# Kernel optimization log

Hardware: AMD Instinct MI355X
Metric: run time of the kernel (lower is better)

The kernel has to match this reference:

```python
import jax, jax.numpy as jnp
import numpy as np

B, T, U, D, V = 8, 128, 64, 512, 1024

def setup_inputs() -> dict:
    key = jax.random.key(0)
    k1, k2, k3, k4, k5, k6 = jax.random.split(key, 6)
    source_encodings = jax.random.normal(k1, (B, T, D), dtype=jnp.float32)
    target_encodings = jax.random.normal(k2, (B, U, D), dtype=jnp.float32)
    source_lengths = jax.random.randint(k3, (B,), 1, T + 1, dtype=jnp.int32)
    target_lengths = jax.random.randint(k4, (B,), 1, U + 1, dtype=jnp.int32)
    # Linear(D, V): weight (V, D), bias (V), init like torch default (uniform)
    bound = 1.0 / np.sqrt(D)
    W = jax.random.uniform(k5, (V, D), minval=-bound, maxval=bound, dtype=jnp.float32)
    b = jax.random.uniform(k6, (V,), minval=-bound, maxval=bound, dtype=jnp.float32)
    return {"source_encodings": source_encodings, "source_lengths": source_lengths,
            "target_encodings": target_encodings, "target_lengths": target_lengths,
            "W": W, "b": b}

def reference(source_encodings, source_lengths, target_encodings, target_lengths, W, b):
    # broadcast add: (B,T,1,D) + (B,1,U,D) -> (B,T,U,D)
    joint = source_encodings[:, :, None, :] + target_encodings[:, None, :, :]
    relu_out = jax.nn.relu(joint)
    # linear projection: (B,T,U,D) x (D,V) + b -> (B,T,U,V)
    output = jnp.einsum('btud,vd->btuv', relu_out, W) + b
    return (output, source_lengths, target_lengths)
```

## Files before the change

### kernel.cpp

```cpp
#include <hip/hip_runtime.h>

typedef unsigned short u16;
typedef float  f32x4  __attribute__((ext_vector_type(4)));
typedef int    i32x4  __attribute__((ext_vector_type(4)));
typedef __bf16 bf16x8 __attribute__((ext_vector_type(8)));

#define AS1 __attribute__((address_space(1)))
#define AS3 __attribute__((address_space(3)))

__device__ __forceinline__ void gload_lds16(const void* g, void* l) {
  __builtin_amdgcn_global_load_lds((AS1 void*)g, (AS3 void*)l, 16, 0, 0);
}

constexpr int B_ = 8, T_ = 128, U_ = 64, D_ = 512, V_ = 1024;
constexpr int M_ = B_ * T_ * U_;

__global__ void prep_all(const float* __restrict__ W,
                         const float* __restrict__ src,
                         const float* __restrict__ tgt,
                         const int* __restrict__ sl, const int* __restrict__ tl,
                         u16* __restrict__ Wb, u16* __restrict__ Aw,
                         float* __restrict__ tail) {
  if (blockIdx.x == 0 && threadIdx.x < 16) {
    const int t = threadIdx.x;
    tail[t] = (t < 8) ? (float)sl[t] : (float)tl[t - 8];
  }
  if (blockIdx.x < 256) {
    const int tid = blockIdx.x * 256 + threadIdx.x;
    const int v  = tid >> 6;
    const int cs = tid & 63;
    const float* sp = W + (size_t)v * D_ + cs * 8;
    float4 w0 = *(const float4*)sp;
    float4 w1 = *(const float4*)(sp + 4);
    union { __bf16 h[8]; i32x4 x; } pk;
    pk.h[0] = (__bf16)w0.x; pk.h[1] = (__bf16)w0.y;
    pk.h[2] = (__bf16)w0.z; pk.h[3] = (__bf16)w0.w;
    pk.h[4] = (__bf16)w1.x; pk.h[5] = (__bf16)w1.y;
    pk.h[6] = (__bf16)w1.z; pk.h[7] = (__bf16)w1.w;
    const int dc = (cs >> 3) * 8 + ((cs & 7) ^ (v & 7));
    *(i32x4*)(Wb + (size_t)v * D_ + dc * 8) = pk.x;
  } else {
    const int tid = (blockIdx.x - 256) * 256 + threadIdx.x;
    const int m  = tid >> 6;
    const int cs = tid & 63;
    const int bt = m >> 6;
    const int u  = m & 63;
    const int b  = m >> 13;
    const float* sp = src + (size_t)bt * D_ + cs * 8;
    const float* tp = tgt + ((size_t)b * U_ + u) * D_ + cs * 8;
    float4 s0 = *(const float4*)sp;
    float4 s1 = *(const float4*)(sp + 4);
    float4 t0 = *(const float4*)tp;
    float4 t1 = *(const float4*)(tp + 4);
    union { __bf16 h[8]; i32x4 x; } pk;
    pk.h[0] = (__bf16)fmaxf(s0.x + t0.x, 0.f);
    pk.h[1] = (__bf16)fmaxf(s0.y + t0.y, 0.f);
    pk.h[2] = (__bf16)fmaxf(s0.z + t0.z, 0.f);
    pk.h[3] = (__bf16)fmaxf(s0.w + t0.w, 0.f);
    pk.h[4] = (__bf16)fmaxf(s1.x + t1.x, 0.f);
    pk.h[5] = (__bf16)fmaxf(s1.y + t1.y, 0.f);
    pk.h[6] = (__bf16)fmaxf(s1.z + t1.z, 0.f);
    pk.h[7] = (__bf16)fmaxf(s1.w + t1.w, 0.f);
    const int dc = (cs >> 3) * 8 + ((cs & 7) ^ (m & 7));
    *(i32x4*)(Aw + (size_t)m * D_ + dc * 8) = pk.x;
  }
}

__global__ void tail_k(const int* __restrict__ sl, const int* __restrict__ tl,
                       float* __restrict__ tail) {
  const int t = threadIdx.x;
  if (t < 8)       tail[t] = (float)sl[t];
  else if (t < 16) tail[t] = (float)tl[t - 8];
}

__global__ __launch_bounds__(256, 2) void joiner_gemm_ws(
    const u16* __restrict__ Aw, const u16* __restrict__ Wb,
    const float* __restrict__ bias, float* __restrict__ out)
{
  __shared__ __align__(16) char As[2][16384];
  __shared__ __align__(16) char Bs[2][16384];

  const int tid  = threadIdx.x;
  const int lane = tid & 63;
  const int wid  = tid >> 6;
  const int wgid = blockIdx.x;
  const int xcd  = wgid & 7;
  const int j    = wgid >> 3;
  const int bm   = xcd * 64 + (j >> 3);
  const int bn   = j & 7;
  const int wm   = (wid >> 1) * 64;
  const int wn   = (wid & 1) * 64;

  f32x4 acc[4][4] = {};

  float bv[4];
  #pragma unroll
  for (int ni = 0; ni < 4; ++ni)
    bv[ni] = bias[bn * 128 + wn + ni * 16 + (lane & 15)];

  auto issueA = [&](int kt, int nb) {
    #pragma unroll
    for (int q = 0; q < 4; ++q) {
      const int i   = wid * 4 + q;
      const int row = i * 8 + (lane >> 3);
      const u16* g = Aw + (size_t)(bm * 128 + row) * D_ + kt * 64 + (lane & 7) * 8;
      gload_lds16(g, As[nb] + i * 1024);
    }
  };
  auto issueB = [&](int kt, int nb) {
    #pragma unroll
    for (int q = 0; q < 4; ++q) {
      const int i   = wid * 4 + q;
      const int row = i * 8 + (lane >> 3);
      const u16* g = Wb + (size_t)(bn * 128 + row) * D_ + kt * 64 + (lane & 7) * 8;
      gload_lds16(g, Bs[nb] + i * 1024);
    }
  };

  auto compute = [&](int cb) {
    #pragma unroll
    for (int s = 0; s < 2; ++s) {
      const int kc = s * 4 + (lane >> 4);
      bf16x8 af[4], bg[4];
      #pragma unroll
      for (int mi = 0; mi < 4; ++mi) {
        const int r = wm + mi * 16 + (lane & 15);
        af[mi] = *(const bf16x8*)(As[cb] + r * 128 + ((kc ^ (r & 7)) << 4));
      }
      #pragma unroll
      for (int ni = 0; ni < 4; ++ni) {
        const int n = wn + ni * 16 + (lane & 15);
        bg[ni] = *(const bf16x8*)(Bs[cb] + n * 128 + ((kc ^ (n & 7)) << 4));
      }
      __builtin_amdgcn_s_setprio(1);
      #pragma unroll
      for (int mi = 0; mi < 4; ++mi)
        #pragma unroll
        for (int ni = 0; ni < 4; ++ni)
          acc[mi][ni] = __builtin_amdgcn_mfma_f32_16x16x32_bf16(
              af[mi], bg[ni], acc[mi][ni], 0, 0, 0);
      __builtin_amdgcn_s_setprio(0);
    }
  };

  issueA(0, 0); issueB(0, 0);

  for (int kt = 0; kt < 8; ++kt) {
    const int cur = kt & 1;
    __syncthreads();
    if (kt < 7) { issueA(kt + 1, cur ^ 1); issueB(kt + 1, cur ^ 1); }
    compute(cur);
  }

  const int col = lane & 15;
  const int r4  = (lane >> 4) * 4;
  #pragma unroll
  for (int mi = 0; mi < 4; ++mi) {
    const size_t mrow = (size_t)bm * 128 + wm + mi * 16 + r4;
    float* op0 = out + mrow * V_ + bn * 128 + wn + col;
    #pragma unroll
    for (int ni = 0; ni < 4; ++ni) {
      float* op = op0 + ni * 16;
      const f32x4 v = acc[mi][ni];
      op[0 * V_] = v[0] + bv[ni];
      op[1 * V_] = v[1] + bv[ni];
      op[2 * V_] = v[2] + bv[ni];
      op[3 * V_] = v[3] + bv[ni];
    }
  }
}

__global__ __launch_bounds__(256, 2) void joiner_gemm_f32(
    const float* __restrict__ src, const float* __restrict__ tgt,
    const float* __restrict__ Wf, const float* __restrict__ bias,
    float* __restrict__ out)
{
  __shared__ char As[128 * 128];
  __shared__ char Bs[128 * 128];

  const int tid  = threadIdx.x;
  const int lane = tid & 63;
  const int wid  = tid >> 6;
  const int bn   = blockIdx.x & 7;
  const int bm   = blockIdx.x >> 3;
  const int bt0  = bm * 2;
  const int bb   = bt0 >> 7;
  const int sr0  = tid >> 3;
  const int sc8  = tid & 7;
  const int wm   = (wid >> 1) * 64;
  const int wn   = (wid & 1) * 64;

  f32x4 acc[4][4] = {};

  const float* srcp0 = src + (size_t)bt0 * D_ + sc8 * 8;
  const float* srcp1 = srcp0 + D_;
  const float* tgtp0 = tgt + ((size_t)bb * U_ + sr0) * D_ + sc8 * 8;
  const float* tgtp1 = tgtp0 + (size_t)32 * D_;

  for (int kt = 0; kt < 8; ++kt) {
    const int k0 = kt * 64;
    #pragma unroll
    for (int jj = 0; jj < 4; ++jj) {
      const int vr = sr0 + 32 * jj;
      const float* wp = Wf + (size_t)(bn * 128 + vr) * D_ + k0 + sc8 * 8;
      float4 w0 = *(const float4*)wp;
      float4 w1 = *(const float4*)(wp + 4);
      union { __bf16 h[8]; i32x4 x; } pk;
      pk.h[0] = (__bf16)w0.x; pk.h[1] = (__bf16)w0.y;
      pk.h[2] = (__bf16)w0.z; pk.h[3] = (__bf16)w0.w;
      pk.h[4] = (__bf16)w1.x; pk.h[5] = (__bf16)w1.y;
      pk.h[6] = (__bf16)w1.z; pk.h[7] = (__bf16)w1.w;
      *(i32x4*)(Bs + vr * 128 + ((sc8 ^ (vr & 7)) << 4)) = pk.x;
    }
    float4 s0a = *(const float4*)(srcp0 + k0), s0b = *(const float4*)(srcp0 + k0 + 4);
    float4 s1a = *(const float4*)(srcp1 + k0), s1b = *(const float4*)(srcp1 + k0 + 4);
    float4 t0a = *(const float4*)(tgtp0 + k0), t0b = *(const float4*)(tgtp0 + k0 + 4);
    float4 t1a = *(const float4*)(tgtp1 + k0), t1b = *(const float4*)(tgtp1 + k0 + 4);
    #pragma unroll
    for (int i = 0; i < 2; ++i) {
      const float4 sa = i ? s1a : s0a;
      const float4 sb = i ? s1b : s0b;
      #pragma unroll
      for (int jj = 0; jj < 2; ++jj) {
        const float4 ta = jj ? t1a : t0a;
        const float4 tb = jj ? t1b : t0b;
        const int r = i * 64 + jj * 32 + sr0;
        union { __bf16 h[8]; i32x4 x; } pk;
        pk.h[0] = (__bf16)fmaxf(sa.x + ta.x, 0.f);
        pk.h[1] = (__bf16)fmaxf(sa.y + ta.y, 0.f);
        pk.h[2] = (__bf16)fmaxf(sa.z + ta.z, 0.f);
        pk.h[3] = (__bf16)fmaxf(sa.w + ta.w, 0.f);
        pk.h[4] = (__bf16)fmaxf(sb.x + tb.x, 0.f);
        pk.h[5] = (__bf16)fmaxf(sb.y + tb.y, 0.f);
        pk.h[6] = (__bf16)fmaxf(sb.z + tb.z, 0.f);
        pk.h[7] = (__bf16)fmaxf(sb.w + tb.w, 0.f);
        *(i32x4*)(As + r * 128 + ((sc8 ^ (r & 7)) << 4)) = pk.x;
      }
    }
    __syncthreads();
    #pragma unroll
    for (int s = 0; s < 2; ++s) {
      const int kc = s * 4 + (lane >> 4);
      bf16x8 af[4], bg[4];
      #pragma unroll
      for (int mi = 0; mi < 4; ++mi) {
        const int r = wm + mi * 16 + (lane & 15);
        af[mi] = *(const bf16x8*)(As + r * 128 + ((kc ^ (r & 7)) << 4));
      }
      #pragma unroll
      for (int ni = 0; ni < 4; ++ni) {
        const int n = wn + ni * 16 + (lane & 15);
        bg[ni] = *(const bf16x8*)(Bs + n * 128 + ((kc ^ (n & 7)) << 4));
      }
      #pragma unroll
      for (int mi = 0; mi < 4; ++mi)
        #pragma unroll
        for (int ni = 0; ni < 4; ++ni)
          acc[mi][ni] = __builtin_amdgcn_mfma_f32_16x16x32_bf16(
              af[mi], bg[ni], acc[mi][ni], 0, 0, 0);
    }
    __syncthreads();
  }

  const int col = lane & 15;
  const int r4  = (lane >> 4) * 4;
  float bv[4];
  #pragma unroll
  for (int ni = 0; ni < 4; ++ni) bv[ni] = bias[bn * 128 + wn + ni * 16 + col];
  #pragma unroll
  for (int mi = 0; mi < 4; ++mi) {
    const size_t mrow = (size_t)bm * 128 + wm + mi * 16 + r4;
    float* op0 = out + mrow * V_ + bn * 128 + wn + col;
    #pragma unroll
    for (int ni = 0; ni < 4; ++ni) {
      float* op = op0 + ni * 16;
      const f32x4 v = acc[mi][ni];
      op[0 * V_] = v[0] + bv[ni];
      op[1 * V_] = v[1] + bv[ni];
      op[2 * V_] = v[2] + bv[ni];
      op[3 * V_] = v[3] + bv[ni];
    }
  }
}

extern "C" void kernel_launch(void* const* d_in, const int* in_sizes, int n_in,
                              void* d_out, int out_size, void* d_ws, size_t ws_size,
                              hipStream_t stream) {
  const float* src  = (const float*)d_in[0];
  const int*   sl   = (const int*)d_in[1];
  const float* tgt  = (const float*)d_in[2];
  const int*   tl   = (const int*)d_in[3];
  const float* W    = (const float*)d_in[4];
  const float* bias = (const float*)d_in[5];
  float* out  = (float*)d_out;
  float* tail = out + (size_t)M_ * V_;

  const size_t needW = (size_t)V_ * D_ * sizeof(u16);
  const size_t needA = (size_t)M_ * D_ * sizeof(u16);

  if (ws_size >= needW + needA) {
    u16* Wb = (u16*)d_ws;
    u16* Aw = Wb + (size_t)V_ * D_;
    prep_all<<<256 + M_ * 64 / 256, 256, 0, stream>>>(W, src, tgt, sl, tl, Wb, Aw, tail);
    joiner_gemm_ws<<<(M_ / 128) * (V_ / 128), 256, 0, stream>>>(Aw, Wb, bias, out);
  } else {
    tail_k<<<1, 64, 0, stream>>>(sl, tl, tail);
    joiner_gemm_f32<<<(M_ / 128) * (V_ / 128), 256, 0, stream>>>(src, tgt, W, bias, out);
  }
}
```

Measured before the change: 116.1 us.

## Fuse broadcast-add ReLU into GEMM A-tile load and widen N tile

Removes the materialized bf16 joint activation buffer (M×D) and instead computes relu(src+tgt) on the fly while filling the A tile in LDS. It also widens each block to 512 threads covering 128×256 output tiles, with the bias folded into the accumulator init. The A/B double buffering is dropped in favour of a single buffer with two barriers per k-step. That saves a large write/read round trip through memory, but loses load/compute overlap and re-reads fp32 src/tgt per tile.

```diff
diff --git a/kernel.cpp b/kernel.cpp
--- a/kernel.cpp
+++ b/kernel.cpp
@@ -15,55 +15,26 @@
 constexpr int B_ = 8, T_ = 128, U_ = 64, D_ = 512, V_ = 1024;
 constexpr int M_ = B_ * T_ * U_;
 
-__global__ void prep_all(const float* __restrict__ W,
-                         const float* __restrict__ src,
-                         const float* __restrict__ tgt,
-                         const int* __restrict__ sl, const int* __restrict__ tl,
-                         u16* __restrict__ Wb, u16* __restrict__ Aw,
-                         float* __restrict__ tail) {
+__global__ void prep_w(const float* __restrict__ W,
+                       const int* __restrict__ sl, const int* __restrict__ tl,
+                       u16* __restrict__ Wb, float* __restrict__ tail) {
   if (blockIdx.x == 0 && threadIdx.x < 16) {
     const int t = threadIdx.x;
     tail[t] = (t < 8) ? (float)sl[t] : (float)tl[t - 8];
   }
-  if (blockIdx.x < 256) {
-    const int tid = blockIdx.x * 256 + threadIdx.x;
-    const int v  = tid >> 6;
-    const int cs = tid & 63;
-    const float* sp = W + (size_t)v * D_ + cs * 8;
-    float4 w0 = *(const float4*)sp;
-    float4 w1 = *(const float4*)(sp + 4);
-    union { __bf16 h[8]; i32x4 x; } pk;
-    pk.h[0] = (__bf16)w0.x; pk.h[1] = (__bf16)w0.y;
-    pk.h[2] = (__bf16)w0.z; pk.h[3] = (__bf16)w0.w;
-    pk.h[4] = (__bf16)w1.x; pk.h[5] = (__bf16)w1.y;
-    pk.h[6] = (__bf16)w1.z; pk.h[7] = (__bf16)w1.w;
-    const int dc = (cs >> 3) * 8 + ((cs & 7) ^ (v & 7));
-    *(i32x4*)(Wb + (size_t)v * D_ + dc * 8) = pk.x;
-  } else {
-    const int tid = (blockIdx.x - 256) * 256 + threadIdx.x;
-    const int m  = tid >> 6;
-    const int cs = tid & 63;
-    const int bt = m >> 6;
-    const int u  = m & 63;
-    const int b  = m >> 13;
-    const float* sp = src + (size_t)bt * D_ + cs * 8;
-    const float* tp = tgt + ((size_t)b * U_ + u) * D_ + cs * 8;
-    float4 s0 = *(const float4*)sp;
-    float4 s1 = *(const float4*)(sp + 4);
-    float4 t0 = *(const float4*)tp;
-    float4 t1 = *(const float4*)(tp + 4);
-    union { __bf16 h[8]; i32x4 x; } pk;
-    pk.h[0] = (__bf16)fmaxf(s0.x + t0.x, 0.f);
-    pk.h[1] = (__bf16)fmaxf(s0.y + t0.y, 0.f);
-    pk.h[2] = (__bf16)fmaxf(s0.z + t0.z, 0.f);
-    pk.h[3] = (__bf16)fmaxf(s0.w + t0.w, 0.f);
-    pk.h[4] = (__bf16)fmaxf(s1.x + t1.x, 0.f);
-    pk.h[5] = (__bf16)fmaxf(s1.y + t1.y, 0.f);
-    pk.h[6] = (__bf16)fmaxf(s1.z + t1.z, 0.f);
-    pk.h[7] = (__bf16)fmaxf(s1.w + t1.w, 0.f);
-    const int dc = (cs >> 3) * 8 + ((cs & 7) ^ (m & 7));
-    *(i32x4*)(Aw + (size_t)m * D_ + dc * 8) = pk.x;
-  }
+  const int tid = blockIdx.x * 256 + threadIdx.x;
+  const int v  = tid >> 6;
+  const int cs = tid & 63;
+  const float* sp = W + (size_t)v * D_ + cs * 8;
+  float4 w0 = *(const float4*)sp;
+  float4 w1 = *(const float4*)(sp + 4);
+  union { __bf16 h[8]; i32x4 x; } pk;
+  pk.h[0] = (__bf16)w0.x; pk.h[1] = (__bf16)w0.y;
+  pk.h[2] = (__bf16)w0.z; pk.h[3] = (__bf16)w0.w;
+  pk.h[4] = (__bf16)w1.x; pk.h[5] = (__bf16)w1.y;
+  pk.h[6] = (__bf16)w1.z; pk.h[7] = (__bf16)w1.w;
+  const int dc = (cs >> 3) * 8 + ((cs & 7) ^ (v & 7));
+  *(i32x4*)(Wb + (size_t)v * D_ + dc * 8) = pk.x;
 }
 
 __global__ void tail_k(const int* __restrict__ sl, const int* __restrict__ tl,
@@ -73,51 +44,91 @@
   else if (t < 16) tail[t] = (float)tl[t - 8];
 }
 
-__global__ __launch_bounds__(256, 2) void joiner_gemm_ws(
-    const u16* __restrict__ Aw, const u16* __restrict__ Wb,
-    const float* __restrict__ bias, float* __restrict__ out)
+__global__ __launch_bounds__(512, 4) void joiner_gemm(
+    const float* __restrict__ src, const float* __restrict__ tgt,
+    const u16* __restrict__ Wb, const float* __restrict__ bias,
+    float* __restrict__ out)
 {
-  __shared__ __align__(16) char As[2][16384];
-  __shared__ __align__(16) char Bs[2][16384];
+  __shared__ __align__(16) char As[16384];
+  __shared__ __align__(16) char Bs[32768];
 
   const int tid  = threadIdx.x;
   const int lane = tid & 63;
   const int wid  = tid >> 6;
   const int wgid = blockIdx.x;
   const int xcd  = wgid & 7;
-  const int j    = wgid >> 3;
-  const int bm   = xcd * 64 + (j >> 3);
-  const int bn   = j & 7;
-  const int wm   = (wid >> 1) * 64;
-  const int wn   = (wid & 1) * 64;
-
-  f32x4 acc[4][4] = {};
-
-  float bv[4];
-  #pragma unroll
-  for (int ni = 0; ni < 4; ++ni)
-    bv[ni] = bias[bn * 128 + wn + ni * 16 + (lane & 15)];
-
-  auto issueA = [&](int kt, int nb) {
-    #pragma unroll
-    for (int q = 0; q < 4; ++q) {
-      const int i   = wid * 4 + q;
-      const int row = i * 8 + (lane >> 3);
-      const u16* g = Aw + (size_t)(bm * 128 + row) * D_ + kt * 64 + (lane & 7) * 8;
-      gload_lds16(g, As[nb] + i * 1024);
-    }
-  };
-  auto issueB = [&](int kt, int nb) {
-    #pragma unroll
-    for (int q = 0; q < 4; ++q) {
-      const int i   = wid * 4 + q;
-      const int row = i * 8 + (lane >> 3);
-      const u16* g = Wb + (size_t)(bn * 128 + row) * D_ + kt * 64 + (lane & 7) * 8;
-      gload_lds16(g, Bs[nb] + i * 1024);
-    }
-  };
-
-  auto compute = [&](int cb) {
+  const int idx  = wgid >> 3;
+  const int bn   = xcd >> 1;
+  const int bmi  = idx * 2 + (xcd & 1);
+  const int bt0  = bmi * 2;
+  const int bb   = bmi >> 6;
+  const int wm   = (wid >> 2) * 64;
+  const int wn   = (wid & 3) * 64;
+
+  f32x4 acc[4][4];
+  #pragma unroll
+  for (int ni = 0; ni < 4; ++ni) {
+    const float bv = bias[bn * 256 + wn + ni * 16 + (lane & 15)];
+    #pragma unroll
+    for (int mi = 0; mi < 4; ++mi) acc[mi][ni] = f32x4{bv, bv, bv, bv};
+  }
+
+  const int r0 = tid >> 2;
+  const int c0 = (tid & 3) * 2;
+  const int bt = bt0 + (r0 >> 6);
+  const int u  = r0 & 63;
+  const float* srcp = src + (size_t)bt * D_ + c0 * 8;
+  const float* tgtp = tgt + ((size_t)bb * U_ + u) * D_ + c0 * 8;
+  char* aw0 = As + r0 * 128 + ((c0 ^ (r0 & 7)) << 4);
+  char* aw1 = As + r0 * 128 + (((c0 + 1) ^ (r0 & 7)) << 4);
+
+  const u16* bbase[4];
+  #pragma unroll
+  for (int q = 0; q < 4; ++q) {
+    const int i   = wid * 4 + q;
+    const int row = i * 8 + (lane >> 3);
+    bbase[q] = Wb + (size_t)(bn * 256 + row) * D_ + (lane & 7) * 8;
+  }
+
+  for (int kt = 0; kt < 8; ++kt) {
+    const int k0 = kt * 64;
+    if (kt > 0) __syncthreads();
+
+    #pragma unroll
+    for (int q = 0; q < 4; ++q)
+      gload_lds16(bbase[q] + k0, Bs + (wid * 4 + q) * 1024);
+
+    {
+      float4 s0 = *(const float4*)(srcp + k0);
+      float4 s1 = *(const float4*)(srcp + k0 + 4);
+      float4 s2 = *(const float4*)(srcp + k0 + 8);
+      float4 s3 = *(const float4*)(srcp + k0 + 12);
+      float4 t0 = *(const float4*)(tgtp + k0);
+      float4 t1 = *(const float4*)(tgtp + k0 + 4);
+      float4 t2 = *(const float4*)(tgtp + k0 + 8);
+      float4 t3 = *(const float4*)(tgtp + k0 + 12);
+      union { __bf16 h[8]; i32x4 x; } pk;
+      pk.h[0] = (__bf16)fmaxf(s0.x + t0.x, 0.f);
+      pk.h[1] = (__bf16)fmaxf(s0.y + t0.y, 0.f);
+      pk.h[2] = (__bf16)fmaxf(s0.z + t0.z, 0.f);
+      pk.h[3] = (__bf16)fmaxf(s0.w + t0.w, 0.f);
+      pk.h[4] = (__bf16)fmaxf(s1.x + t1.x, 0.f);
+      pk.h[5] = (__bf16)fmaxf(s1.y + t1.y, 0.f);
+      pk.h[6] = (__bf16)fmaxf(s1.z + t1.z, 0.f);
+      pk.h[7] = (__bf16)fmaxf(s1.w + t1.w, 0.f);
+      *(i32x4*)aw0 = pk.x;
+      pk.h[0] = (__bf16)fmaxf(s2.x + t2.x, 0.f);
+      pk.h[1] = (__bf16)fmaxf(s2.y + t2.y, 0.f);
+      pk.h[2] = (__bf16)fmaxf(s2.z + t2.z, 0.f);
+      pk.h[3] = (__bf16)fmaxf(s2.w + t2.w, 0.f);
+      pk.h[4] = (__bf16)fmaxf(s3.x + t3.x, 0.f);
+      pk.h[5] = (__bf16)fmaxf(s3.y + t3.y, 0.f);
+      pk.h[6] = (__bf16)fmaxf(s3.z + t3.z, 0.f);
+      pk.h[7] = (__bf16)fmaxf(s3.w + t3.w, 0.f);
+      *(i32x4*)aw1 = pk.x;
+    }
+    __syncthreads();
+
     #pragma unroll
     for (int s = 0; s < 2; ++s) {
       const int kc = s * 4 + (lane >> 4);
@@ -125,12 +136,12 @@
       #pragma unroll
       for (int mi = 0; mi < 4; ++mi) {
         const int r = wm + mi * 16 + (lane & 15);
-        af[mi] = *(const bf16x8*)(As[cb] + r * 128 + ((kc ^ (r & 7)) << 4));
+        af[mi] = *(const bf16x8*)(As + r * 128 + ((kc ^ (r & 7)) << 4));
       }
       #pragma unroll
       for (int ni = 0; ni < 4; ++ni) {
         const int n = wn + ni * 16 + (lane & 15);
-        bg[ni] = *(const bf16x8*)(Bs[cb] + n * 128 + ((kc ^ (n & 7)) << 4));
+        bg[ni] = *(const bf16x8*)(Bs + n * 128 + ((kc ^ (n & 7)) << 4));
       }
       __builtin_amdgcn_s_setprio(1);
       #pragma unroll
@@ -141,31 +152,22 @@
               af[mi], bg[ni], acc[mi][ni], 0, 0, 0);
       __builtin_amdgcn_s_setprio(0);
     }
-  };
-
-  issueA(0, 0); issueB(0, 0);
-
-  for (int kt = 0; kt < 8; ++kt) {
-    const int cur = kt & 1;
-    __syncthreads();
-    if (kt < 7) { issueA(kt + 1, cur ^ 1); issueB(kt + 1, cur ^ 1); }
-    compute(cur);
   }
 
   const int col = lane & 15;
   const int r4  = (lane >> 4) * 4;
   #pragma unroll
   for (int mi = 0; mi < 4; ++mi) {
-    const size_t mrow = (size_t)bm * 128 + wm + mi * 16 + r4;
-    float* op0 = out + mrow * V_ + bn * 128 + wn + col;
+    const size_t mrow = (size_t)bmi * 128 + wm + mi * 16 + r4;
+    float* op0 = out + mrow * V_ + bn * 256 + wn + col;
     #pragma unroll
     for (int ni = 0; ni < 4; ++ni) {
       float* op = op0 + ni * 16;
       const f32x4 v = acc[mi][ni];
-      op[0 * V_] = v[0] + bv[ni];
-      op[1 * V_] = v[1] + bv[ni];
-      op[2 * V_] = v[2] + bv[ni];
-      op[3 * V_] = v[3] + bv[ni];
+      op[0 * V_] = v[0];
+      op[1 * V_] = v[1];
+      op[2 * V_] = v[2];
+      op[3 * V_] = v[3];
     }
   }
 }
@@ -295,16 +297,14 @@
   float* out  = (float*)d_out;
   float* tail = out + (size_t)M_ * V_;
 
-  const size_t needW = (size_t)V_ * D_ * sizeof(u16);
-  const size_t needA = (size_t)M_ * D_ * sizeof(u16);
-
-  if (ws_size >= needW + needA) {
+  if (ws_size >= (size_t)V_ * D_ * sizeof(u16)) {
     u16* Wb = (u16*)d_ws;
-    u16* Aw = Wb + (size_t)V_ * D_;
-    prep_all<<<256 + M_ * 64 / 256, 256, 0, stream>>>(W, src, tgt, sl, tl, Wb, Aw, tail);
-    joiner_gemm_ws<<<(M_ / 128) * (V_ / 128), 256, 0, stream>>>(Aw, Wb, bias, out);
+    prep_w<<<256, 256, 0, stream>>>(W, sl, tl, Wb, tail);
+    joiner_gemm<<<(M_ / 128) * (V_ / 256), 512, 0, stream>>>(
+        src, tgt, Wb, bias, out);
   } else {
     tail_k<<<1, 64, 0, stream>>>(sl, tl, tail);
-    joiner_gemm_f32<<<(M_ / 128) * (V_ / 128), 256, 0, stream>>>(src, tgt, W, bias, out);
-  }
-}
+    joiner_gemm_f32<<<(M_ / 128) * (V_ / 128), 256, 0, stream>>>(
+        src, tgt, W, bias, out);
+  }
+}
```

After: 137.4 us. 1.18x slower.

## Fuse broadcast-add ReLU expansion into GEMM A-tile loading instead of materializing

Applied to the files above, without the earlier changes.

Removes the materialized bf16 joint activation buffer (M×D) and instead builds each A tile inside the GEMM from src and tgt rows: registers are prefetched, added, ReLU'd, converted to bf16 and written into a single-buffered swizzled LDS tile. The prep kernel now only converts W. Occupancy is raised to 3 blocks per CU, and block-to-tile mapping drops the XCD-aware swizzle. This avoids writing and rereading a 64 MB intermediate, at the cost of extra barriers, VALU work in the main loop, and a single-buffered A tile that serializes expansion and compute.

```diff
diff --git a/kernel.cpp b/kernel.cpp
--- a/kernel.cpp
+++ b/kernel.cpp
@@ -15,55 +15,26 @@
 constexpr int B_ = 8, T_ = 128, U_ = 64, D_ = 512, V_ = 1024;
 constexpr int M_ = B_ * T_ * U_;
 
-__global__ void prep_all(const float* __restrict__ W,
-                         const float* __restrict__ src,
-                         const float* __restrict__ tgt,
-                         const int* __restrict__ sl, const int* __restrict__ tl,
-                         u16* __restrict__ Wb, u16* __restrict__ Aw,
-                         float* __restrict__ tail) {
+__global__ void prep_w(const float* __restrict__ W,
+                       const int* __restrict__ sl, const int* __restrict__ tl,
+                       u16* __restrict__ Wb, float* __restrict__ tail) {
   if (blockIdx.x == 0 && threadIdx.x < 16) {
     const int t = threadIdx.x;
     tail[t] = (t < 8) ? (float)sl[t] : (float)tl[t - 8];
   }
-  if (blockIdx.x < 256) {
-    const int tid = blockIdx.x * 256 + threadIdx.x;
-    const int v  = tid >> 6;
-    const int cs = tid & 63;
-    const float* sp = W + (size_t)v * D_ + cs * 8;
-    float4 w0 = *(const float4*)sp;
-    float4 w1 = *(const float4*)(sp + 4);
-    union { __bf16 h[8]; i32x4 x; } pk;
-    pk.h[0] = (__bf16)w0.x; pk.h[1] = (__bf16)w0.y;
-    pk.h[2] = (__bf16)w0.z; pk.h[3] = (__bf16)w0.w;
-    pk.h[4] = (__bf16)w1.x; pk.h[5] = (__bf16)w1.y;
-    pk.h[6] = (__bf16)w1.z; pk.h[7] = (__bf16)w1.w;
-    const int dc = (cs >> 3) * 8 + ((cs & 7) ^ (v & 7));
-    *(i32x4*)(Wb + (size_t)v * D_ + dc * 8) = pk.x;
-  } else {
-    const int tid = (blockIdx.x - 256) * 256 + threadIdx.x;
-    const int m  = tid >> 6;
-    const int cs = tid & 63;
-    const int bt = m >> 6;
-    const int u  = m & 63;
-    const int b  = m >> 13;
-    const float* sp = src + (size_t)bt * D_ + cs * 8;
-    const float* tp = tgt + ((size_t)b * U_ + u) * D_ + cs * 8;
-    float4 s0 = *(const float4*)sp;
-    float4 s1 = *(const float4*)(sp + 4);
-    float4 t0 = *(const float4*)tp;
-    float4 t1 = *(const float4*)(tp + 4);
-    union { __bf16 h[8]; i32x4 x; } pk;
-    pk.h[0] = (__bf16)fmaxf(s0.x + t0.x, 0.f);
-    pk.h[1] = (__bf16)fmaxf(s0.y + t0.y, 0.f);
-    pk.h[2] = (__bf16)fmaxf(s0.z + t0.z, 0.f);
-    pk.h[3] = (__bf16)fmaxf(s0.w + t0.w, 0.f);
-    pk.h[4] = (__bf16)fmaxf(s1.x + t1.x, 0.f);
-    pk.h[5] = (__bf16)fmaxf(s1.y + t1.y, 0.f);
-    pk.h[6] = (__bf16)fmaxf(s1.z + t1.z, 0.f);
-    pk.h[7] = (__bf16)fmaxf(s1.w + t1.w, 0.f);
-    const int dc = (cs >> 3) * 8 + ((cs & 7) ^ (m & 7));
-    *(i32x4*)(Aw + (size_t)m * D_ + dc * 8) = pk.x;
-  }
+  const int tid = blockIdx.x * 256 + threadIdx.x;
+  const int v  = tid >> 6;
+  const int cs = tid & 63;
+  const float* sp = W + (size_t)v * D_ + cs * 8;
+  float4 w0 = *(const float4*)sp;
+  float4 w1 = *(const float4*)(sp + 4);
+  union { __bf16 h[8]; i32x4 x; } pk;
+  pk.h[0] = (__bf16)w0.x; pk.h[1] = (__bf16)w0.y;
+  pk.h[2] = (__bf16)w0.z; pk.h[3] = (__bf16)w0.w;
+  pk.h[4] = (__bf16)w1.x; pk.h[5] = (__bf16)w1.y;
+  pk.h[6] = (__bf16)w1.z; pk.h[7] = (__bf16)w1.w;
+  const int dc = (cs >> 3) * 8 + ((cs & 7) ^ (v & 7));
+  *(i32x4*)(Wb + (size_t)v * D_ + dc * 8) = pk.x;
 }
 
 __global__ void tail_k(const int* __restrict__ sl, const int* __restrict__ tl,
@@ -73,47 +44,82 @@
   else if (t < 16) tail[t] = (float)tl[t - 8];
 }
 
-__global__ __launch_bounds__(256, 2) void joiner_gemm_ws(
-    const u16* __restrict__ Aw, const u16* __restrict__ Wb,
-    const float* __restrict__ bias, float* __restrict__ out)
+__global__ __launch_bounds__(256, 3) void joiner_gemm(
+    const float* __restrict__ src, const float* __restrict__ tgt,
+    const u16* __restrict__ Wb, const float* __restrict__ bias,
+    float* __restrict__ out)
 {
-  __shared__ __align__(16) char As[2][16384];
+  __shared__ __align__(16) char As[16384];
   __shared__ __align__(16) char Bs[2][16384];
 
   const int tid  = threadIdx.x;
   const int lane = tid & 63;
   const int wid  = tid >> 6;
-  const int wgid = blockIdx.x;
-  const int xcd  = wgid & 7;
-  const int j    = wgid >> 3;
-  const int bm   = xcd * 64 + (j >> 3);
-  const int bn   = j & 7;
+  const int bn   = blockIdx.x & 7;
+  const int bm   = blockIdx.x >> 3;
+  const int bt0  = bm * 2;
+  const int bb   = bt0 >> 7;
+  const int sr0  = tid >> 3;
+  const int sc8  = tid & 7;
   const int wm   = (wid >> 1) * 64;
   const int wn   = (wid & 1) * 64;
 
   f32x4 acc[4][4] = {};
 
+  const float* srcp0 = src + (size_t)bt0 * D_ + sc8 * 8;
+  const float* srcp1 = srcp0 + D_;
+  const float* tgtp0 = tgt + ((size_t)bb * U_ + sr0) * D_ + sc8 * 8;
+  const float* tgtp1 = tgtp0 + (size_t)32 * D_;
+
   float bv[4];
   #pragma unroll
   for (int ni = 0; ni < 4; ++ni)
     bv[ni] = bias[bn * 128 + wn + ni * 16 + (lane & 15)];
 
-  auto issueA = [&](int kt, int nb) {
-    #pragma unroll
-    for (int q = 0; q < 4; ++q) {
-      const int i   = wid * 4 + q;
-      const int row = i * 8 + (lane >> 3);
-      const u16* g = Aw + (size_t)(bm * 128 + row) * D_ + kt * 64 + (lane & 7) * 8;
-      gload_lds16(g, As[nb] + i * 1024);
-    }
+  const u16* bbase[4];
+  #pragma unroll
+  for (int q = 0; q < 4; ++q) {
+    const int i   = wid * 4 + q;
+    const int row = i * 8 + (lane >> 3);
+    bbase[q] = Wb + (size_t)(bn * 128 + row) * D_ + (lane & 7) * 8;
+  }
+
+  float4 pS0a, pS0b, pS1a, pS1b, pT0a, pT0b, pT1a, pT1b;
+
+  auto loadA = [&](int kt) {
+    const int k0 = kt * 64;
+    pS0a = *(const float4*)(srcp0 + k0); pS0b = *(const float4*)(srcp0 + k0 + 4);
+    pS1a = *(const float4*)(srcp1 + k0); pS1b = *(const float4*)(srcp1 + k0 + 4);
+    pT0a = *(const float4*)(tgtp0 + k0); pT0b = *(const float4*)(tgtp0 + k0 + 4);
+    pT1a = *(const float4*)(tgtp1 + k0); pT1b = *(const float4*)(tgtp1 + k0 + 4);
   };
   auto issueB = [&](int kt, int nb) {
     #pragma unroll
-    for (int q = 0; q < 4; ++q) {
-      const int i   = wid * 4 + q;
-      const int row = i * 8 + (lane >> 3);
-      const u16* g = Wb + (size_t)(bn * 128 + row) * D_ + kt * 64 + (lane & 7) * 8;
-      gload_lds16(g, Bs[nb] + i * 1024);
+    for (int q = 0; q < 4; ++q)
+      gload_lds16(bbase[q] + kt * 64, Bs[nb] + (wid * 4 + q) * 1024);
+  };
+
+  auto expandA = [&]() {
+    #pragma unroll
+    for (int i = 0; i < 2; ++i) {
+      const float4 sa = i ? pS1a : pS0a;
+      const float4 sb = i ? pS1b : pS0b;
+      #pragma unroll
+      for (int j = 0; j < 2; ++j) {
+        const float4 ta = j ? pT1a : pT0a;
+        const float4 tb = j ? pT1b : pT0b;
+        const int r = i * 64 + j * 32 + sr0;
+        union { __bf16 h[8]; i32x4 x; } pk;
+        pk.h[0] = (__bf16)fmaxf(sa.x + ta.x, 0.f);
+        pk.h[1] = (__bf16)fmaxf(sa.y + ta.y, 0.f);
+        pk.h[2] = (__bf16)fmaxf(sa.z + ta.z, 0.f);
+        pk.h[3] = (__bf16)fmaxf(sa.w + ta.w, 0.f);
+        pk.h[4] = (__bf16)fmaxf(sb.x + tb.x, 0.f);
+        pk.h[5] = (__bf16)fmaxf(sb.y + tb.y, 0.f);
+        pk.h[6] = (__bf16)fmaxf(sb.z + tb.z, 0.f);
+        pk.h[7] = (__bf16)fmaxf(sb.w + tb.w, 0.f);
+        *(i32x4*)(As + r * 128 + ((sc8 ^ (r & 7)) << 4)) = pk.x;
+      }
     }
   };
 
@@ -125,7 +131,7 @@
       #pragma unroll
       for (int mi = 0; mi < 4; ++mi) {
         const int r = wm + mi * 16 + (lane & 15);
-        af[mi] = *(const bf16x8*)(As[cb] + r * 128 + ((kc ^ (r & 7)) << 4));
+        af[mi] = *(const bf16x8*)(As + r * 128 + ((kc ^ (r & 7)) << 4));
       }
       #pragma unroll
       for (int ni = 0; ni < 4; ++ni) {
@@ -143,13 +149,30 @@
     }
   };
 
-  issueA(0, 0); issueB(0, 0);
+  loadA(0);
+  issueB(0, 0);
+  expandA();
+  asm volatile("s_waitcnt vmcnt(0) lgkmcnt(0)" ::: "memory");
+  __builtin_amdgcn_sched_barrier(0);
+  __builtin_amdgcn_s_barrier();
+  __builtin_amdgcn_sched_barrier(0);
 
   for (int kt = 0; kt < 8; ++kt) {
-    const int cur = kt & 1;
-    __syncthreads();
-    if (kt < 7) { issueA(kt + 1, cur ^ 1); issueB(kt + 1, cur ^ 1); }
-    compute(cur);
+    if (kt < 7) {
+      loadA(kt + 1);
+      issueB(kt + 1, (kt + 1) & 1);
+    }
+    __builtin_amdgcn_sched_barrier(0);
+    compute(kt & 1);
+    if (kt < 7) {
+      __builtin_amdgcn_sched_barrier(0);
+      __builtin_amdgcn_s_barrier();
+      expandA();
+      asm volatile("s_waitcnt vmcnt(0) lgkmcnt(0)" ::: "memory");
+      __builtin_amdgcn_sched_barrier(0);
+      __builtin_amdgcn_s_barrier();
+      __builtin_amdgcn_sched_barrier(0);
+    }
   }
 
   const int col = lane & 15;
@@ -295,16 +318,14 @@
   float* out  = (float*)d_out;
   float* tail = out + (size_t)M_ * V_;
 
-  const size_t needW = (size_t)V_ * D_ * sizeof(u16);
-  const size_t needA = (size_t)M_ * D_ * sizeof(u16);
-
-  if (ws_size >= needW + needA) {
+  if (ws_size >= (size_t)V_ * D_ * sizeof(u16)) {
     u16* Wb = (u16*)d_ws;
-    u16* Aw = Wb + (size_t)V_ * D_;
-    prep_all<<<256 + M_ * 64 / 256, 256, 0, stream>>>(W, src, tgt, sl, tl, Wb, Aw, tail);
-    joiner_gemm_ws<<<(M_ / 128) * (V_ / 128), 256, 0, stream>>>(Aw, Wb, bias, out);
+    prep_w<<<256, 256, 0, stream>>>(W, sl, tl, Wb, tail);
+    joiner_gemm<<<(M_ / 128) * (V_ / 128), 256, 0, stream>>>(
+        src, tgt, Wb, bias, out);
   } else {
     tail_k<<<1, 64, 0, stream>>>(sl, tl, tail);
-    joiner_gemm_f32<<<(M_ / 128) * (V_ / 128), 256, 0, stream>>>(src, tgt, W, bias, out);
-  }
-}
+    joiner_gemm_f32<<<(M_ / 128) * (V_ / 128), 256, 0, stream>>>(
+        src, tgt, W, bias, out);
+  }
+}
```

Result: faster. 105.1 us (-9.4%).
